# Optimization experiments

Hardware: AMD Instinct MI355X
Metric: run time of the kernel (lower is better)

The kernel has to match this reference:

```python
import jax, jax.numpy as jnp
import numpy as np

SQRT3 = 3.0 ** 0.5


def setup_inputs() -> dict:
    key = jax.random.key(0)
    k1, k2 = jax.random.split(key)
    N, M, D = 8192, 4096, 64
    X = jax.random.normal(k1, (N, D), dtype=jnp.float32)
    Z = jax.random.normal(k2, (M, D), dtype=jnp.float32)
    sigma = jnp.asarray(1.0, dtype=jnp.float32)
    lengthscale = jnp.asarray(2.0, dtype=jnp.float32)
    return {"X": X, "Z": Z, "sigma": sigma, "lengthscale": lengthscale}


def reference(X, Z, sigma, lengthscale):
    # Pairwise squared distances via GEMM expansion (avoids [N,M,D] diff tensor).
    x2 = jnp.sum(X * X, axis=-1)[:, None]            # [N,1]
    z2 = jnp.sum(Z * Z, axis=-1)[None, :]            # [1,M]
    sq = x2 + z2 - 2.0 * jnp.einsum('nd,md->nm', X, Z)  # [N,M]
    dist = jnp.sqrt(jnp.maximum(sq, 1e-12))
    val = SQRT3 * dist / lengthscale
    return (sigma ** 2) * (1.0 + val) * jnp.exp(-val)  # [N,M] Matern-3/2 Gram
```

## Files before the change

### kernel.cpp

```cpp
#include <hip/hip_runtime.h>
#include <math.h>

#define SQRT3F 1.7320508075688772f

typedef _Float16 half8 __attribute__((ext_vector_type(8)));
typedef _Float16 half4 __attribute__((ext_vector_type(4)));
typedef float    f32x4 __attribute__((ext_vector_type(4)));


__global__ __launch_bounds__(256)
void matern_prep_kernel(const float* __restrict__ X, const float* __restrict__ Z,
                        _Float16* __restrict__ Xh, _Float16* __restrict__ Xl,
                        _Float16* __restrict__ Zh, _Float16* __restrict__ Zl,
                        float* __restrict__ x2, float* __restrict__ z2,
                        int N, int M) {
    int f = blockIdx.x * 256 + threadIdx.x;
    const int totX = N * 16;
    const int tot  = (N + M) * 16;
    if (f >= tot) return;
    const float* src; _Float16 *dh, *dl; float* nrm;
    if (f < totX) { src = X; dh = Xh; dl = Xl; nrm = x2; }
    else          { f -= totX; src = Z; dh = Zh; dl = Zl; nrm = z2; }

    float4 v = *(const float4*)(src + (size_t)f * 4);
    _Float16 hx = (_Float16)v.x, hy = (_Float16)v.y, hz = (_Float16)v.z, hw = (_Float16)v.w;
    half4 hv = { hx, hy, hz, hw };
    half4 lv = { (_Float16)(v.x - (float)hx), (_Float16)(v.y - (float)hy),
                 (_Float16)(v.z - (float)hz), (_Float16)(v.w - (float)hw) };
    *(half4*)(dh + (size_t)f * 4) = hv;
    *(half4*)(dl + (size_t)f * 4) = lv;

    float ssq = v.x * v.x + v.y * v.y + v.z * v.z + v.w * v.w;
    ssq += __shfl_xor(ssq, 1, 16);
    ssq += __shfl_xor(ssq, 2, 16);
    ssq += __shfl_xor(ssq, 4, 16);
    ssq += __shfl_xor(ssq, 8, 16);
    if ((threadIdx.x & 15) == 0) nrm[f >> 4] = ssq;
}

__global__ __launch_bounds__(256, 4)
void matern_main_kernel(const _Float16* __restrict__ Xh, const _Float16* __restrict__ Xl,
                        const _Float16* __restrict__ Zh, const _Float16* __restrict__ Zl,
                        const float* __restrict__ x2, const float* __restrict__ z2,
                        const float* __restrict__ sigma, const float* __restrict__ lengthscale,
                        float* __restrict__ out, int M) {
    const int t    = threadIdx.x;
    const int lane = t & 63;
    const int w    = t >> 6;
    const int wr   = w >> 1;
    const int wc   = w & 1;
    const int m0   = blockIdx.y * 128 + wr * 64;
    const int n0   = blockIdx.x * 64  + wc * 32;
    const int lm   = lane & 15;
    const int q    = lane >> 4;

    f32x4 acc[4][2];
    #pragma unroll
    for (int a = 0; a < 4; ++a)
        #pragma unroll
        for (int b = 0; b < 2; ++b)
            acc[a][b] = (f32x4){0.f, 0.f, 0.f, 0.f};

    #pragma unroll
    for (int kc = 0; kc < 2; ++kc) {
        const int k = kc * 32 + q * 8;
        half8 ah[4], al[4], bh[2], bl[2];
        #pragma unroll
        for (int mt = 0; mt < 4; ++mt) {
            const int off = (m0 + mt * 16 + lm) * 64 + k;
            ah[mt] = *(const half8*)(Xh + off);
            al[mt] = *(const half8*)(Xl + off);
        }
        #pragma unroll
        for (int nt = 0; nt < 2; ++nt) {
            const int off = (n0 + nt * 16 + lm) * 64 + k;
            bh[nt] = *(const half8*)(Zh + off);
            bl[nt] = *(const half8*)(Zl + off);
        }
        #pragma unroll
        for (int mt = 0; mt < 4; ++mt)
            #pragma unroll
            for (int nt = 0; nt < 2; ++nt) {
                acc[mt][nt] = __builtin_amdgcn_mfma_f32_16x16x32_f16(ah[mt], bh[nt], acc[mt][nt], 0, 0, 0);
                acc[mt][nt] = __builtin_amdgcn_mfma_f32_16x16x32_f16(ah[mt], bl[nt], acc[mt][nt], 0, 0, 0);
                acc[mt][nt] = __builtin_amdgcn_mfma_f32_16x16x32_f16(al[mt], bh[nt], acc[mt][nt], 0, 0, 0);
            }
    }

    const float s   = sigma[0];
    const float l   = lengthscale[0];
    const float fac = SQRT3F / l;
    const float s2  = s * s;

    #pragma unroll
    for (int mt = 0; mt < 4; ++mt) {
        const int row0 = m0 + mt * 16 + q * 4;
        const f32x4 xr = *(const f32x4*)(x2 + row0);
        #pragma unroll
        for (int nt = 0; nt < 2; ++nt) {
            const int col = n0 + nt * 16 + lm;
            const float zc = z2[col];
            float* op = out + (size_t)row0 * (size_t)M + col;
            #pragma unroll
            for (int r = 0; r < 4; ++r) {
                float sq  = xr[r] + zc - 2.0f * acc[mt][nt][r];
                float d   = __builtin_amdgcn_sqrtf(fmaxf(sq, 1e-12f));
                float val = fac * d;
                __builtin_nontemporal_store(s2 * (1.0f + val) * __expf(-val), op);
                op += M;
            }
        }
    }
}

extern "C" void kernel_launch(void* const* d_in, const int* in_sizes, int n_in,
                              void* d_out, int out_size, void* d_ws, size_t ws_size,
                              hipStream_t stream) {
    (void)n_in; (void)out_size; (void)ws_size;
    const float* X   = (const float*)d_in[0];
    const float* Z   = (const float*)d_in[1];
    const float* sig = (const float*)d_in[2];
    const float* len = (const float*)d_in[3];
    float* out = (float*)d_out;

    const int D = 64;
    const int N = in_sizes[0] / D;
    const int M = in_sizes[1] / D;

    char* ws = (char*)d_ws;
    size_t o = 0;
    auto take = [&](size_t bytes) { char* p = ws + o; o += (bytes + 255) & ~(size_t)255; return p; };
    _Float16* Xh = (_Float16*)take((size_t)N * D * sizeof(_Float16));
    _Float16* Xl = (_Float16*)take((size_t)N * D * sizeof(_Float16));
    _Float16* Zh = (_Float16*)take((size_t)M * D * sizeof(_Float16));
    _Float16* Zl = (_Float16*)take((size_t)M * D * sizeof(_Float16));
    float*    x2 = (float*)take((size_t)N * sizeof(float));
    float*    z2 = (float*)take((size_t)M * sizeof(float));

    const int tot = (N + M) * 16;
    matern_prep_kernel<<<(tot + 255) / 256, 256, 0, stream>>>(X, Z, Xh, Xl, Zh, Zl, x2, z2, N, M);

    dim3 grid(M / 64, N / 128);
    matern_main_kernel<<<grid, 256, 0, stream>>>(Xh, Xl, Zh, Zl, x2, z2, sig, len, out, M);
}
```

Before: 184.0 us.

## Pre-swizzle fp16 split operands into MFMA fragment order; use plain output stores

The prep kernel now writes the hi/lo fp16 halves of X and Z in a blocked layout matching the per-lane MFMA fragment order, so each wave's half8 loads in the main kernel become fully contiguous 1KB chunks instead of strided row reads. The row-norm computation moves to a separate set of threads in the same prep launch. The output store also switches from nontemporal to a regular store. The cost is a more complex prep indexing scheme and extra prep threads. The output is a 128MB write-bound stream, so the store change may matter more than the load layout.

After: 150.5 us (median of 2 runs). 1.22x faster.

```diff
diff --git a/kernel.cpp b/kernel.cpp
--- a/kernel.cpp
+++ b/kernel.cpp
@@ -14,28 +14,50 @@
                         _Float16* __restrict__ Zh, _Float16* __restrict__ Zl,
                         float* __restrict__ x2, float* __restrict__ z2,
                         int N, int M) {
-    int f = blockIdx.x * 256 + threadIdx.x;
-    const int totX = N * 16;
-    const int tot  = (N + M) * 16;
-    if (f >= tot) return;
-    const float* src; _Float16 *dh, *dl; float* nrm;
-    if (f < totX) { src = X; dh = Xh; dl = Xl; nrm = x2; }
-    else          { f -= totX; src = Z; dh = Zh; dl = Zl; nrm = z2; }
+    const int idx    = blockIdx.x * 256 + threadIdx.x;
+    const int cellsX = N * 8;
+    const int cells  = (N + M) * 8;
 
-    float4 v = *(const float4*)(src + (size_t)f * 4);
-    _Float16 hx = (_Float16)v.x, hy = (_Float16)v.y, hz = (_Float16)v.z, hw = (_Float16)v.w;
-    half4 hv = { hx, hy, hz, hw };
-    half4 lv = { (_Float16)(v.x - (float)hx), (_Float16)(v.y - (float)hy),
-                 (_Float16)(v.z - (float)hz), (_Float16)(v.w - (float)hw) };
-    *(half4*)(dh + (size_t)f * 4) = hv;
-    *(half4*)(dl + (size_t)f * 4) = lv;
-
-    float ssq = v.x * v.x + v.y * v.y + v.z * v.z + v.w * v.w;
-    ssq += __shfl_xor(ssq, 1, 16);
-    ssq += __shfl_xor(ssq, 2, 16);
-    ssq += __shfl_xor(ssq, 4, 16);
-    ssq += __shfl_xor(ssq, 8, 16);
-    if ((threadIdx.x & 15) == 0) nrm[f >> 4] = ssq;
+    if (idx < cells) {
+        const float* src; _Float16 *dh, *dl; int c = idx;
+        if (c < cellsX) { src = X; dh = Xh; dl = Xl; }
+        else            { c -= cellsX; src = Z; dh = Zh; dl = Zl; }
+        const int R   = c >> 7;
+        const int w_  = c & 127;
+        const int kc  = w_ >> 6;
+        const int q   = (w_ >> 4) & 3;
+        const int lm  = w_ & 15;
+        const int row = R * 16 + lm;
+        const int k   = kc * 32 + q * 8;
+        const float* p = src + (size_t)row * 64 + k;
+        const float4 a = *(const float4*)p;
+        const float4 b = *(const float4*)(p + 4);
+        const float in[8] = { a.x, a.y, a.z, a.w, b.x, b.y, b.z, b.w };
+        half8 hv, lv;
+        #pragma unroll
+        for (int j = 0; j < 8; ++j) {
+            _Float16 h = (_Float16)in[j];
+            hv[j] = h;
+            lv[j] = (_Float16)(in[j] - (float)h);
+        }
+        *(half8*)(dh + (size_t)c * 8) = hv;
+        *(half8*)(dl + (size_t)c * 8) = lv;
+    } else {
+        int f = idx - cells;
+        const int totX = N * 16;
+        const int tot  = (N + M) * 16;
+        if (f >= tot) return;
+        const float* src; float* nrm;
+        if (f < totX) { src = X; nrm = x2; }
+        else          { f -= totX; src = Z; nrm = z2; }
+        const float4 v = *(const float4*)(src + (size_t)f * 4);
+        float ssq = v.x * v.x + v.y * v.y + v.z * v.z + v.w * v.w;
+        ssq += __shfl_xor(ssq, 1, 16);
+        ssq += __shfl_xor(ssq, 2, 16);
+        ssq += __shfl_xor(ssq, 4, 16);
+        ssq += __shfl_xor(ssq, 8, 16);
+        if ((threadIdx.x & 15) == 0) nrm[f >> 4] = ssq;
+    }
 }
 
 __global__ __launch_bounds__(256, 4)
@@ -51,6 +73,8 @@
     const int wc   = w & 1;
     const int m0   = blockIdx.y * 128 + wr * 64;
     const int n0   = blockIdx.x * 64  + wc * 32;
+    const int Rb0  = (blockIdx.y * 8) + wr * 4;
+    const int Cb0  = (blockIdx.x * 4) + wc * 2;
     const int lm   = lane & 15;
     const int q    = lane >> 4;
 
@@ -63,17 +87,16 @@
 
     #pragma unroll
     for (int kc = 0; kc < 2; ++kc) {
-        const int k = kc * 32 + q * 8;
         half8 ah[4], al[4], bh[2], bl[2];
         #pragma unroll
         for (int mt = 0; mt < 4; ++mt) {
-            const int off = (m0 + mt * 16 + lm) * 64 + k;
+            const size_t off = ((size_t)(Rb0 + mt) * 2 + kc) * 512 + (size_t)lane * 8;
             ah[mt] = *(const half8*)(Xh + off);
             al[mt] = *(const half8*)(Xl + off);
         }
         #pragma unroll
         for (int nt = 0; nt < 2; ++nt) {
-            const int off = (n0 + nt * 16 + lm) * 64 + k;
+            const size_t off = ((size_t)(Cb0 + nt) * 2 + kc) * 512 + (size_t)lane * 8;
             bh[nt] = *(const half8*)(Zh + off);
             bl[nt] = *(const half8*)(Zl + off);
         }
@@ -106,7 +129,7 @@
                 float sq  = xr[r] + zc - 2.0f * acc[mt][nt][r];
                 float d   = __builtin_amdgcn_sqrtf(fmaxf(sq, 1e-12f));
                 float val = fac * d;
-                __builtin_nontemporal_store(s2 * (1.0f + val) * __expf(-val), op);
+                *op = s2 * (1.0f + val) * __expf(-val);
                 op += M;
             }
         }
@@ -137,7 +160,8 @@
     float*    x2 = (float*)take((size_t)N * sizeof(float));
     float*    z2 = (float*)take((size_t)M * sizeof(float));
 
-    const int tot = (N + M) * 16;
+    const int cells = (N + M) * 8;
+    const int tot   = cells + (N + M) * 16;
     matern_prep_kernel<<<(tot + 255) / 256, 256, 0, stream>>>(X, Z, Xh, Xl, Zh, Zl, x2, z2, N, M);
 
     dim3 grid(M / 64, N / 128);
```
